# Performance work log

Hardware: AMD Instinct MI355X
Metric: run time of the kernel (lower is better)

Reference implementation:

```python
import jax, jax.numpy as jnp
import numpy as np

B, T, D_IN, H = 2048, 240, 180, 90


def setup_inputs() -> dict:
    key = jax.random.key(0)
    k1, k2, k3, k4, k5 = jax.random.split(key, 5)
    s = 1.0 / np.sqrt(H)  # torch LSTMCell init scale
    return {
        "x": jax.random.normal(k1, (B, 3, 60, 240), dtype=jnp.float32),
        "W_ih": jax.random.uniform(k2, (4 * H, D_IN), dtype=jnp.float32, minval=-s, maxval=s),
        "W_hh": jax.random.uniform(k3, (4 * H, H), dtype=jnp.float32, minval=-s, maxval=s),
        "b_ih": jax.random.uniform(k4, (4 * H,), dtype=jnp.float32, minval=-s, maxval=s),
        "b_hh": jax.random.uniform(k5, (4 * H,), dtype=jnp.float32, minval=-s, maxval=s),
    }


def reference(x, W_ih, W_hh, b_ih, b_hh):
    # (B, 3, 60, 240) -> (B, 240, 3, 60) -> (B, 240, 180)
    b = x.shape[0]
    xt = jnp.transpose(x, (0, 3, 1, 2)).reshape(b, T, D_IN)
    # NOTE: the torch module calls LSTMCell without carrying state, so h0=c0=0
    # at EVERY timestep; the W_hh contribution is identically zero and all
    # timesteps are independent -> one batched GEMM over (B*T).
    gates = jnp.einsum("bti,gi->btg", xt, W_ih) + b_ih + b_hh  # (B, T, 4H)
    i_g, f_g, g_g, o_g = jnp.split(gates, 4, axis=-1)  # torch gate order i,f,g,o
    c = jax.nn.sigmoid(i_g) * jnp.tanh(g_g)  # f_g * c_prev = 0
    h = jax.nn.sigmoid(o_g) * jnp.tanh(c)
    return jax.nn.sigmoid(h)  # (B, T, H)
```

## Files before the change

kernel.cpp:

```cpp
#include <hip/hip_runtime.h>


#define B_SZ 2048
#define T_SZ 240
#define K_SZ 180
#define H_SZ 90
#define KP   192
#define TB   80
#define NP   3
#define NTT  5

#define WS_B_OFF 110592

typedef __bf16 bf16x8 __attribute__((ext_vector_type(8)));
typedef __bf16 bf16x4 __attribute__((ext_vector_type(4)));
typedef float  f32x4  __attribute__((ext_vector_type(4)));

__device__ __forceinline__ float sigmoidf_(float x) {
    return __builtin_amdgcn_rcpf(1.0f + __expf(-x));
}
__device__ __forceinline__ float tanhf_(float x) {
    return 1.0f - 2.0f * __builtin_amdgcn_rcpf(__expf(2.0f * x) + 1.0f);
}

__device__ __forceinline__ int skey(int t) {
    return (2 * (t + (t >> 4))) & 14;
}
__device__ __forceinline__ int sgran(int g, int t) {
    return (g & ~15) | ((g ^ skey(t)) & 15);
}

__global__ __launch_bounds__(384) void prepack_kernel(
    const float* __restrict__ W_ih,
    const float* __restrict__ b_ih,
    const float* __restrict__ b_hh,
    void* __restrict__ ws)
{
    __bf16* wp = (__bf16*)ws;
    float*  bp = (float*)((char*)ws + WS_B_OFF);
    const int gb[3] = {0, 180, 270};

    const int bid = blockIdx.x;
    const int tid = threadIdx.x;
    if (bid < 18) {
        const int g  = bid / 6;
        const int ks = bid % 6;
        const int w  = tid >> 6;
        const int l  = tid & 63;
        const int q  = l >> 4;
        const int n  = l & 15;
        const int h  = w * 16 + n;
        bf16x8 f;
        #pragma unroll
        for (int j = 0; j < 8; ++j) {
            int k = ks * 32 + q * 8 + j;
            float v = (h < H_SZ && k < K_SZ) ? W_ih[(size_t)(gb[g] + h) * K_SZ + k] : 0.0f;
            f[j] = (__bf16)v;
        }
        *(bf16x8*)(wp + (size_t)(((g * 6 + ks) * 6 + w) * 64 + l) * 8) = f;
    } else {
        if (tid < 288) {
            int g = tid / 96, hh = tid % 96;
            bp[g * 96 + hh] = (hh < H_SZ) ? (b_ih[gb[g] + hh] + b_hh[gb[g] + hh]) : 0.0f;
        }
    }
}

__global__ __launch_bounds__(384)
__attribute__((amdgpu_waves_per_eu(3, 3)))
void lstm_fused_kernel(
    const float* __restrict__ x,
    const void*  __restrict__ ws,
    float* __restrict__ out)
{
    __shared__ __align__(16) __bf16 aBuf[TB * KP];

    const int bid  = blockIdx.x;
    const int b    = bid / NP;
    const int part = bid - b * NP;
    const int t0   = part * TB;

    const int tid  = threadIdx.x;
    const int wave = tid >> 6;
    const int lane = tid & 63;
    const int q    = lane >> 4;
    const int n    = lane & 15;
    const int h    = wave * 16 + n;
    const bool hv  = (h < H_SZ);

    const float* xb = x + (size_t)b * (K_SZ * T_SZ) + t0;

    const int k4a = tid / 20,         t4a = tid - (tid / 20) * 20;
    const int k4b = (tid + 384) / 20, t4b = (tid + 384) - ((tid + 384) / 20) * 20;
    const int k4c = (tid + 768) / 20, t4c = (tid + 768) - ((tid + 768) / 20) * 20;
    const bool u2v = (tid < 132);

    f32x4 r0[4], r1[4], r2[4];
    {
        const float* sa = xb + (k4a * 4) * T_SZ + t4a * 4;
        const float* sb = xb + (k4b * 4) * T_SZ + t4b * 4;
        const float* sc = xb + (k4c * 4) * T_SZ + t4c * 4;
        #pragma unroll
        for (int r = 0; r < 4; ++r) r0[r] = *(const f32x4*)(sa + r * T_SZ);
        #pragma unroll
        for (int r = 0; r < 4; ++r) r1[r] = *(const f32x4*)(sb + r * T_SZ);
        if (u2v) {
            #pragma unroll
            for (int r = 0; r < 4; ++r) r2[r] = *(const f32x4*)(sc + r * T_SZ);
        }
    }

    const bf16x8* wp = (const bf16x8*)ws;
    bf16x8 bfrag[3][6];
    #pragma unroll
    for (int g = 0; g < 3; ++g)
        #pragma unroll
        for (int ks = 0; ks < 6; ++ks)
            bfrag[g][ks] = wp[((g * 6 + ks) * 6 + wave) * 64 + lane];

    const float* bp = (const float*)((const char*)ws + WS_B_OFF);
    const float bias_i = bp[0 * 96 + h];
    const float bias_g = bp[1 * 96 + h];
    const float bias_o = bp[2 * 96 + h];
    float* ob = out + (size_t)b * (T_SZ * H_SZ) + (size_t)t0 * H_SZ;

    if (tid < TB * 3) {
        int t  = tid / 3;
        int gz = 45 + (tid - (tid / 3) * 3);
        *(unsigned long long*)(aBuf + t * KP + sgran(gz, t) * 4) = 0ull;
    }

#define WRITEU(R, K4, T4)                                               \
    {                                                                   \
        _Pragma("unroll")                                               \
        for (int j = 0; j < 4; ++j) {                                   \
            int t = (T4) * 4 + j;                                       \
            bf16x4 w;                                                   \
            w[0] = (__bf16)R[0][j]; w[1] = (__bf16)R[1][j];             \
            w[2] = (__bf16)R[2][j]; w[3] = (__bf16)R[3][j];             \
            *(bf16x4*)(aBuf + t * KP + sgran((K4), t) * 4) = w;         \
        }                                                               \
    }
    WRITEU(r0, k4a, t4a);
    WRITEU(r1, k4b, t4b);
    if (u2v) WRITEU(r2, k4c, t4c);
#undef WRITEU

    __syncthreads();

    #pragma unroll
    for (int tt = 0; tt < NTT; ++tt) {
        f32x4 acc0 = {0.f, 0.f, 0.f, 0.f};
        f32x4 acc1 = {0.f, 0.f, 0.f, 0.f};
        f32x4 acc2 = {0.f, 0.f, 0.f, 0.f};
        const int t = tt * 16 + n;
        #pragma unroll
        for (int ks = 0; ks < 6; ++ks) {
            int g = ks * 8 + 2 * q;
            bf16x8 a = *(const bf16x8*)(aBuf + t * KP + sgran(g, t) * 4);
            acc0 = __builtin_amdgcn_mfma_f32_16x16x32_bf16(a, bfrag[0][ks], acc0, 0, 0, 0);
            acc1 = __builtin_amdgcn_mfma_f32_16x16x32_bf16(a, bfrag[1][ks], acc1, 0, 0, 0);
            acc2 = __builtin_amdgcn_mfma_f32_16x16x32_bf16(a, bfrag[2][ks], acc2, 0, 0, 0);
        }
        if (hv) {
            const int tg = tt * 16 + q * 4;
            #pragma unroll
            for (int e = 0; e < 4; ++e) {
                float gi = acc0[e] + bias_i;
                float gg = acc1[e] + bias_g;
                float go = acc2[e] + bias_o;
                float cc = sigmoidf_(gi) * tanhf_(gg);
                float hh = sigmoidf_(go) * tanhf_(cc);
                ob[(size_t)(tg + e) * H_SZ + h] = sigmoidf_(hh);
            }
        }
        if (tt + 1 < NTT) __builtin_amdgcn_s_barrier();
    }
}

extern "C" void kernel_launch(void* const* d_in, const int* in_sizes, int n_in,
                              void* d_out, int out_size, void* d_ws, size_t ws_size,
                              hipStream_t stream) {
    const float* x    = (const float*)d_in[0];
    const float* W_ih = (const float*)d_in[1];
    const float* b_ih = (const float*)d_in[3];
    const float* b_hh = (const float*)d_in[4];
    float* out = (float*)d_out;

    prepack_kernel<<<dim3(19), dim3(384), 0, stream>>>(W_ih, b_ih, b_hh, d_ws);
    lstm_fused_kernel<<<dim3(B_SZ * NP), dim3(384), 0, stream>>>(x, d_ws, out);
}
```

Before: 595.0 us.

## Restructure LSTM kernel into single-wave blocks per 16-timestep tile with bias folded into GEMM

```diff
diff --git a/kernel.cpp b/kernel.cpp
--- a/kernel.cpp
+++ b/kernel.cpp
@@ -6,11 +6,8 @@
 #define K_SZ 180
 #define H_SZ 90
 #define KP   192
-#define TB   80
-#define NP   3
-#define NTT  5
-
-#define WS_B_OFF 110592
+#define TT   16
+#define NMT  15
 
 typedef __bf16 bf16x8 __attribute__((ext_vector_type(8)));
 typedef __bf16 bf16x4 __attribute__((ext_vector_type(4)));
@@ -23,11 +20,8 @@
     return 1.0f - 2.0f * __builtin_amdgcn_rcpf(__expf(2.0f * x) + 1.0f);
 }
 
-__device__ __forceinline__ int skey(int t) {
-    return (2 * (t + (t >> 4))) & 14;
-}
-__device__ __forceinline__ int sgran(int g, int t) {
-    return (g & ~15) | ((g ^ skey(t)) & 15);
+__device__ __forceinline__ int sg16(int g, int t) {
+    return (g & ~15) | ((g ^ ((2 * t) & 14)) & 15);
 }
 
 __global__ __launch_bounds__(384) void prepack_kernel(
@@ -37,63 +31,50 @@
     void* __restrict__ ws)
 {
     __bf16* wp = (__bf16*)ws;
-    float*  bp = (float*)((char*)ws + WS_B_OFF);
     const int gb[3] = {0, 180, 270};
 
     const int bid = blockIdx.x;
     const int tid = threadIdx.x;
-    if (bid < 18) {
-        const int g  = bid / 6;
-        const int ks = bid % 6;
-        const int w  = tid >> 6;
-        const int l  = tid & 63;
-        const int q  = l >> 4;
-        const int n  = l & 15;
-        const int h  = w * 16 + n;
-        bf16x8 f;
-        #pragma unroll
-        for (int j = 0; j < 8; ++j) {
-            int k = ks * 32 + q * 8 + j;
-            float v = (h < H_SZ && k < K_SZ) ? W_ih[(size_t)(gb[g] + h) * K_SZ + k] : 0.0f;
-            f[j] = (__bf16)v;
+    const int g  = bid / 6;
+    const int ks = bid % 6;
+    const int w  = tid >> 6;
+    const int l  = tid & 63;
+    const int q  = l >> 4;
+    const int n  = l & 15;
+    const int h  = w * 16 + n;
+    bf16x8 f;
+    #pragma unroll
+    for (int j = 0; j < 8; ++j) {
+        int k = ks * 32 + q * 8 + j;
+        float v = 0.0f;
+        if (h < H_SZ) {
+            if (k < K_SZ)       v = W_ih[(size_t)(gb[g] + h) * K_SZ + k];
+            else if (k == K_SZ) v = b_ih[gb[g] + h] + b_hh[gb[g] + h];
         }
-        *(bf16x8*)(wp + (size_t)(((g * 6 + ks) * 6 + w) * 64 + l) * 8) = f;
-    } else {
-        if (tid < 288) {
-            int g = tid / 96, hh = tid % 96;
-            bp[g * 96 + hh] = (hh < H_SZ) ? (b_ih[gb[g] + hh] + b_hh[gb[g] + hh]) : 0.0f;
-        }
+        f[j] = (__bf16)v;
     }
+    *(bf16x8*)(wp + (size_t)(((g * 6 + ks) * 6 + w) * 64 + l) * 8) = f;
 }
 
-__global__ __launch_bounds__(384)
-__attribute__((amdgpu_waves_per_eu(3, 3)))
-void lstm_fused_kernel(
+__global__ __launch_bounds__(64, 4) void lstm_fused_kernel(
     const float* __restrict__ x,
     const void*  __restrict__ ws,
     float* __restrict__ out)
 {
-    __shared__ __align__(16) __bf16 aBuf[TB * KP];
+    __shared__ __align__(16) __bf16 aBuf[TT * KP];
 
-    const int bid  = blockIdx.x;
-    const int b    = bid / NP;
-    const int part = bid - b * NP;
-    const int t0   = part * TB;
-
-    const int tid  = threadIdx.x;
-    const int wave = tid >> 6;
-    const int lane = tid & 63;
+    const int lane = threadIdx.x;
     const int q    = lane >> 4;
     const int n    = lane & 15;
-    const int h    = wave * 16 + n;
-    const bool hv  = (h < H_SZ);
+    const int mt   = blockIdx.x;
+    const int b    = blockIdx.y;
 
-    const float* xb = x + (size_t)b * (K_SZ * T_SZ) + t0;
+    const float* xb = x + (size_t)b * (K_SZ * T_SZ) + mt * TT;
 
-    const int k4a = tid / 20,         t4a = tid - (tid / 20) * 20;
-    const int k4b = (tid + 384) / 20, t4b = (tid + 384) - ((tid + 384) / 20) * 20;
-    const int k4c = (tid + 768) / 20, t4c = (tid + 768) - ((tid + 768) / 20) * 20;
-    const bool u2v = (tid < 132);
+    const int k4a = lane >> 2,        t4a = lane & 3;
+    const int k4b = (lane + 64) >> 2, t4b = t4a;
+    const int k4c = (lane + 128) >> 2, t4c = t4a;
+    const bool cv = (lane < 52);
 
     f32x4 r0[4], r1[4], r2[4];
     {
@@ -101,33 +82,20 @@
         const float* sb = xb + (k4b * 4) * T_SZ + t4b * 4;
         const float* sc = xb + (k4c * 4) * T_SZ + t4c * 4;
         #pragma unroll
-        for (int r = 0; r < 4; ++r) r0[r] = *(const f32x4*)(sa + r * T_SZ);
+        for (int j = 0; j < 4; ++j) r0[j] = *(const f32x4*)(sa + j * T_SZ);
         #pragma unroll
-        for (int r = 0; r < 4; ++r) r1[r] = *(const f32x4*)(sb + r * T_SZ);
-        if (u2v) {
+        for (int j = 0; j < 4; ++j) r1[j] = *(const f32x4*)(sb + j * T_SZ);
+        if (cv) {
             #pragma unroll
-            for (int r = 0; r < 4; ++r) r2[r] = *(const f32x4*)(sc + r * T_SZ);
+            for (int j = 0; j < 4; ++j) r2[j] = *(const f32x4*)(sc + j * T_SZ);
         }
     }
 
-    const bf16x8* wp = (const bf16x8*)ws;
-    bf16x8 bfrag[3][6];
-    #pragma unroll
-    for (int g = 0; g < 3; ++g)
-        #pragma unroll
-        for (int ks = 0; ks < 6; ++ks)
-            bfrag[g][ks] = wp[((g * 6 + ks) * 6 + wave) * 64 + lane];
-
-    const float* bp = (const float*)((const char*)ws + WS_B_OFF);
-    const float bias_i = bp[0 * 96 + h];
-    const float bias_g = bp[1 * 96 + h];
-    const float bias_o = bp[2 * 96 + h];
-    float* ob = out + (size_t)b * (T_SZ * H_SZ) + (size_t)t0 * H_SZ;
-
-    if (tid < TB * 3) {
-        int t  = tid / 3;
-        int gz = 45 + (tid - (tid / 3) * 3);
-        *(unsigned long long*)(aBuf + t * KP + sgran(gz, t) * 4) = 0ull;
+    if (lane < 48) {
+        int t  = lane / 3;
+        int gz = 45 + (lane - (lane / 3) * 3);
+        unsigned long long v = (gz == 45) ? 0x3F80ull : 0ull;
+        *(unsigned long long*)(&aBuf[t * KP + sg16(gz, t) * 4]) = v;
     }
 
 #define WRITEU(R, K4, T4)                                               \
@@ -138,43 +106,51 @@
             bf16x4 w;                                                   \
             w[0] = (__bf16)R[0][j]; w[1] = (__bf16)R[1][j];             \
             w[2] = (__bf16)R[2][j]; w[3] = (__bf16)R[3][j];             \
-            *(bf16x4*)(aBuf + t * KP + sgran((K4), t) * 4) = w;         \
+            *(bf16x4*)(&aBuf[t * KP + sg16((K4), t) * 4]) = w;          \
         }                                                               \
     }
     WRITEU(r0, k4a, t4a);
     WRITEU(r1, k4b, t4b);
-    if (u2v) WRITEU(r2, k4c, t4c);
+    if (cv) WRITEU(r2, k4c, t4c);
 #undef WRITEU
 
-    __syncthreads();
+    const bf16x8* wp = (const bf16x8*)ws;
+    f32x4 acc[6][3];
+    #pragma unroll
+    for (int ht = 0; ht < 6; ++ht)
+        #pragma unroll
+        for (int g = 0; g < 3; ++g)
+            acc[ht][g] = (f32x4){0.f, 0.f, 0.f, 0.f};
 
     #pragma unroll
-    for (int tt = 0; tt < NTT; ++tt) {
-        f32x4 acc0 = {0.f, 0.f, 0.f, 0.f};
-        f32x4 acc1 = {0.f, 0.f, 0.f, 0.f};
-        f32x4 acc2 = {0.f, 0.f, 0.f, 0.f};
-        const int t = tt * 16 + n;
+    for (int ks = 0; ks < 6; ++ks) {
+        bf16x8 a = *(const bf16x8*)(&aBuf[n * KP + sg16(ks * 8 + 2 * q, n) * 4]);
         #pragma unroll
-        for (int ks = 0; ks < 6; ++ks) {
-            int g = ks * 8 + 2 * q;
-            bf16x8 a = *(const bf16x8*)(aBuf + t * KP + sgran(g, t) * 4);
-            acc0 = __builtin_amdgcn_mfma_f32_16x16x32_bf16(a, bfrag[0][ks], acc0, 0, 0, 0);
-            acc1 = __builtin_amdgcn_mfma_f32_16x16x32_bf16(a, bfrag[1][ks], acc1, 0, 0, 0);
-            acc2 = __builtin_amdgcn_mfma_f32_16x16x32_bf16(a, bfrag[2][ks], acc2, 0, 0, 0);
+        for (int ht = 0; ht < 6; ++ht) {
+            bf16x8 w0 = wp[((0 * 6 + ks) * 6 + ht) * 64 + lane];
+            bf16x8 w1 = wp[((1 * 6 + ks) * 6 + ht) * 64 + lane];
+            bf16x8 w2 = wp[((2 * 6 + ks) * 6 + ht) * 64 + lane];
+            acc[ht][0] = __builtin_amdgcn_mfma_f32_16x16x32_bf16(a, w0, acc[ht][0], 0, 0, 0);
+            acc[ht][1] = __builtin_amdgcn_mfma_f32_16x16x32_bf16(a, w1, acc[ht][1], 0, 0, 0);
+            acc[ht][2] = __builtin_amdgcn_mfma_f32_16x16x32_bf16(a, w2, acc[ht][2], 0, 0, 0);
         }
-        if (hv) {
-            const int tg = tt * 16 + q * 4;
-            #pragma unroll
-            for (int e = 0; e < 4; ++e) {
-                float gi = acc0[e] + bias_i;
-                float gg = acc1[e] + bias_g;
-                float go = acc2[e] + bias_o;
-                float cc = sigmoidf_(gi) * tanhf_(gg);
-                float hh = sigmoidf_(go) * tanhf_(cc);
-                ob[(size_t)(tg + e) * H_SZ + h] = sigmoidf_(hh);
-            }
+    }
+
+    float* ob = out + (size_t)b * (T_SZ * H_SZ) + (size_t)(mt * TT) * H_SZ;
+    #pragma unroll
+    for (int ht = 0; ht < 6; ++ht) {
+        const int  h  = ht * 16 + n;
+        const bool hv = (h < H_SZ);
+        #pragma unroll
+        for (int e = 0; e < 4; ++e) {
+            float gi = acc[ht][0][e];
+            float gg = acc[ht][1][e];
+            float go = acc[ht][2][e];
+            float cc = sigmoidf_(gi) * tanhf_(gg);
+            float hh = sigmoidf_(go) * tanhf_(cc);
+            float v  = sigmoidf_(hh);
+            if (hv) ob[(size_t)(q * 4 + e) * H_SZ + h] = v;
         }
-        if (tt + 1 < NTT) __builtin_amdgcn_s_barrier();
     }
 }
 
@@ -187,6 +163,6 @@
     const float* b_hh = (const float*)d_in[4];
     float* out = (float*)d_out;
 
-    prepack_kernel<<<dim3(19), dim3(384), 0, stream>>>(W_ih, b_ih, b_hh, d_ws);
-    lstm_fused_kernel<<<dim3(B_SZ * NP), dim3(384), 0, stream>>>(x, d_ws, out);
+    prepack_kernel<<<dim3(18), dim3(384), 0, stream>>>(W_ih, b_ih, b_hh, d_ws);
+    lstm_fused_kernel<<<dim3(NMT, B_SZ), dim3(64), 0, stream>>>(x, d_ws, out);
 }
```

After: 672.6 us. 13.1% more time.
